# Kernel tuning notes

Measured on AMD Instinct MI355X. Metric: run time of the kernel, lower is better.

The kernel has to match this reference:

```python
import jax, jax.numpy as jnp
import numpy as np
import math


def _fft_size(n: int) -> int:
    return max(2 * 2 ** int(math.ceil(math.log2(n))), 16)


def setup_inputs() -> dict:
    key = jax.random.key(0)
    k1, k2 = jax.random.split(key)
    b, n, d = 4, 8192, 512
    x = jax.random.normal(k1, (b, n, d), dtype=jnp.float32)
    t = jax.random.normal(k2, (n, d), dtype=jnp.float32)
    return {"x": x, "t": t}


def reference(x, t):
    # x: (b, n, d); t: (n, d) Toeplitz coefficients t0..t_{n-1} per channel.
    # o[b, i, d] = gelu( sum_{j<=i} t[i-j, d] * x[b, j, d] )
    # computed via zero-padded real FFT of size >= 2n (causal linear conv).
    b, n, d = x.shape
    N = _fft_size(n)  # 2 * next_pow2(n)
    t_f = jnp.fft.rfft(t, n=N, axis=0)          # (N//2+1, d) complex
    x_f = jnp.fft.rfft(x, n=N, axis=1)          # (b, N//2+1, d) complex
    y = jnp.fft.irfft(x_f * t_f[None], n=N, axis=1)[:, :n, :]  # (b, n, d)
    return jax.nn.gelu(y)
```

## Files before the change

### kernel.cpp

```cpp
#include <hip/hip_runtime.h>
#include <hip/hip_bf16.h>

typedef short short8 __attribute__((ext_vector_type(8)));
typedef float f32x4  __attribute__((ext_vector_type(4)));

#define N_SEQ 8192
#define D_CH  512

constexpr int XSLOTS  = 1280;
constexpr int XLDS_B  = XSLOTS * 8;
constexpr int TSTRIDE = 272;
constexpr int TLDS_B  = 8 * TSTRIDE;
constexpr int ALL_LDS = XLDS_B + TLDS_B;

__device__ __forceinline__ unsigned short f32_to_bf16_bits(float f) {
    union { float f; unsigned int u; } v; v.f = f;
    unsigned int u = v.u;
    unsigned int r = u + 0x7FFFu + ((u >> 16) & 1u);
    return (unsigned short)(r >> 16);
}

__device__ __forceinline__ float gelu_f(float v) {
  float w = v * (2.3022031f + 0.10294296f * v * v);
  float e = __builtin_amdgcn_exp2f(w);
  float r = __builtin_amdgcn_rcpf(e + 1.0f);
  return v - v * r;
}

__global__ __launch_bounds__(256) void transpose_cast_kernel(
    const float* __restrict__ x, const float* __restrict__ t,
    unsigned short* __restrict__ xT, unsigned short* __restrict__ tT) {
  __shared__ float tile[64][65];
  int blk = blockIdx.x;
  int bat = blk >> 10;
  int rem = blk & 1023;
  int i0 = (rem >> 3) << 6;
  int d0 = (rem & 7) << 6;
  const float* src; unsigned short* dst;
  if (bat < 4) { src = x + (size_t)bat * N_SEQ * D_CH; dst = xT + (size_t)bat * D_CH * N_SEQ; }
  else         { src = t;                              dst = tT; }
  int tx = threadIdx.x & 63, ty = threadIdx.x >> 6;
  #pragma unroll
  for (int r = ty; r < 64; r += 4)
    tile[r][tx] = src[(size_t)(i0 + r) * D_CH + (d0 + tx)];
  __syncthreads();
  #pragma unroll
  for (int r = ty; r < 64; r += 4)
    dst[(size_t)(d0 + r) * N_SEQ + (i0 + tx)] = f32_to_bf16_bits(tile[tx][r]);
}

__global__ __launch_bounds__(256) void transpose_out_kernel(
    const float* __restrict__ src, float* __restrict__ dst) {
  __shared__ float tile[64][65];
  int blk = blockIdx.x;
  int b   = blk >> 10;
  int rem = blk & 1023;
  int d0 = (rem & 7) << 6;
  int i0 = (rem >> 3) << 6;
  int tx = threadIdx.x & 63, ty = threadIdx.x >> 6;
  #pragma unroll
  for (int r = ty; r < 64; r += 4)
    tile[r][tx] = src[((size_t)(d0 + r) * 4 + b) * N_SEQ + i0 + tx];
  __syncthreads();
  #pragma unroll
  for (int r = ty; r < 64; r += 4)
    dst[((size_t)b * N_SEQ + i0 + r) * D_CH + d0 + tx] = tile[tx][r];
}

template<int DMAJOR>
__global__ __launch_bounds__(64, 3) void tno_conv_kernel(
    const unsigned short* __restrict__ xT, const unsigned short* __restrict__ tT,
    float* __restrict__ outp) {
  __shared__ __align__(16) char lds[ALL_LDS];
  const int lane = threadIdx.x & 63;
  const int blk  = blockIdx.x;
  const int d    = blk & 511;
  const int strip = 7 - (blk >> 9);
  const int base  = strip << 10;
  const int l_hi  = base + 960;

  const int m      = lane & 15;
  const int kb     = (lane >> 4) << 3;
  const int bcol   = m & 3;
  const int sl     = m >> 2;
  const int rA     = m & 7;
  const int aConst = kb - (m & 8);
  char* ldsX = lds;
  char* ldsT = lds + XLDS_B;
  const char* tb = ldsT + rA * TSTRIDE;
  const int stJ  = lane & 31;
  const int stR0 = (lane >> 5) << 2;
  const unsigned short* tTd = tT + ((size_t)d << 13);
  const int uLin = (lane & 3) | ((lane >> 4) << 2);
  const int sb   = (lane >> 2) & 3;
  const unsigned short* xlaneB = xT + (((size_t)sb * D_CH + d) << 13) + (uLin << 1);

  typedef __attribute__((address_space(3))) unsigned int lds_u32;
  typedef const __attribute__((address_space(1))) unsigned int glb_u32;

  f32x4 acc[4][4];
  #pragma unroll
  for (int g = 0; g < 4; ++g)
    #pragma unroll
    for (int k = 0; k < 4; ++k)
      acc[g][k] = (f32x4){0.f, 0.f, 0.f, 0.f};

  unsigned short tp0 = tTd[l_hi + 32 + stJ];
  unsigned short tp1 = tTd[l_hi + stJ];
  unsigned short tp2 = tTd[l_hi - 32 + stJ];
  asm volatile("" ::: "memory");

  {
    f32x4 z = (f32x4){0.f, 0.f, 0.f, 0.f};
    #pragma unroll
    for (int j = 0; j < 7; ++j)
      *(f32x4*)(ldsX + 2560 + (j << 10) + (lane << 4)) = z;
    *(unsigned long long*)(ldsX + 9728 + (lane << 3)) = 0ull;
    #pragma unroll
    for (int j = 0; j < 8; ++j)
      __builtin_amdgcn_global_load_lds((glb_u32*)(const void*)(xlaneB + (j << 5)),
                                       (lds_u32*)(void*)(ldsX + (j << 8)), 4, 0, 0);
  }
  asm volatile("" ::: "memory");

  #pragma unroll
  for (int c = 0; c < 4; ++c) {
    int r = stR0 + c;
    char* cw = ldsT + r * TSTRIDE;
    *(unsigned short*)(cw + (((r - (l_hi + 32 + stJ)) & 127) << 1)) = tp0;
    *(unsigned short*)(cw + (((r - (l_hi      + stJ)) & 127) << 1)) = tp1;
    *(unsigned short*)(cw + (((r - (l_hi - 32 + stJ)) & 127) << 1)) = tp2;
  }

  unsigned short tv[8];
  #pragma unroll
  for (int u = 0; u < 8; ++u)
    tv[u] = tTd[l_hi - 32 * u - 63 + stJ];

  asm volatile("s_waitcnt vmcnt(0)" ::: "memory");

  int aC = ((aConst - l_hi) & 127) << 1;
  short8 af2 = *(const short8*)(tb + ((aC - 64) & 255));
  short8 af3 = *(const short8*)(tb + ((aC - 96) & 255));
  int xo[4];
  #pragma unroll
  for (int g = 0; g < 4; ++g) {
    int row = (base - l_hi) + (g << 8) + (sl << 6) + kb;
    int slot = row + ((row < 0) ? XSLOTS : 0);
    xo[g] = (slot << 3) + (bcol << 4);
  }
  int twb[4];
  #pragma unroll
  for (int c = 0; c < 4; ++c)
    twb[c] = (((stR0 + c) - (l_hi - 63 + stJ)) & 127) << 1;
  int tgi = l_hi - 319 + stJ;
  const unsigned short* xsp = xlaneB + 256;
  int wb = 256 << 3;

#define CONV_ITER(GMIN, U)                                                       \
  {                                                                              \
    asm volatile("s_waitcnt vmcnt(14)" ::: "memory");                            \
    short8 af0 = *(const short8*)(tb + aC);                                      \
    short8 af1 = *(const short8*)(tb + ((aC - 32) & 255));                       \
    __builtin_amdgcn_global_load_lds((glb_u32*)(const void*)xsp,                 \
        (lds_u32*)(void*)(ldsX + wb), 4, 0, 0);                                  \
    __builtin_amdgcn_s_setprio(1);                                               \
    _Pragma("unroll")                                                            \
    for (int g = 0; g < 4; ++g) {                                                \
      if (g >= (GMIN)) {                                                         \
        short8 bf = *(const short8*)(ldsX + xo[g]);                              \
        acc[g][0] = __builtin_amdgcn_mfma_f32_16x16x32_bf16(af0, bf, acc[g][0], 0, 0, 0); \
        acc[g][1] = __builtin_amdgcn_mfma_f32_16x16x32_bf16(af1, bf, acc[g][1], 0, 0, 0); \
        acc[g][2] = __builtin_amdgcn_mfma_f32_16x16x32_bf16(af2, bf, acc[g][2], 0, 0, 0); \
        acc[g][3] = __builtin_amdgcn_mfma_f32_16x16x32_bf16(af3, bf, acc[g][3], 0, 0, 0); \
      }                                                                          \
      xo[g] += 256; if (xo[g] >= XLDS_B) xo[g] -= XLDS_B;                        \
    }                                                                            \
    __builtin_amdgcn_s_setprio(0);                                               \
    { unsigned short tvs = tv[U];                                                \
      _Pragma("unroll")                                                          \
      for (int c = 0; c < 4; ++c) {                                              \
        *(unsigned short*)(ldsT + (stR0 + c) * TSTRIDE + twb[c]) = tvs;          \
        twb[c] = (twb[c] + 64) & 255;                                            \
      }                                                                          \
    }                                                                            \
    { int ti = (tgi < 0) ? 0 : tgi;                                              \
      unsigned short v = tTd[ti];               \
      tv[U] = (tgi < 0) ? (unsigned short)0 : v;                                 \
      tgi -= 32; }                                                               \
    af2 = af0; af3 = af1;                                                        \
    aC = (aC + 64) & 255;                                                        \
    xsp += 32;                                                                   \
    wb += 256; if (wb >= XLDS_B) wb -= XLDS_B;                                   \
  }

#define PH8(GMIN)                                                                \
    { _Pragma("unroll")                                                          \
      for (int u = 0; u < 8; ++u) CONV_ITER(GMIN, u) }

  PH8(3)
  PH8(2)
  PH8(1)
  const int n0 = (strip << 2) + 1;
  #pragma unroll 1
  for (int c8 = 0; c8 < n0; ++c8)
    PH8(0)
#undef PH8
#undef CONV_ITER

  asm volatile("s_waitcnt vmcnt(0)" ::: "memory");

  if (DMAJOR) {
    float* op = outp + ((((size_t)d << 2) + bcol) << 13) + base + (sl << 6) + ((lane >> 4) << 2);
    #pragma unroll
    for (int g = 0; g < 4; ++g)
      #pragma unroll
      for (int k = 0; k < 4; ++k)
        #pragma unroll
        for (int r = 0; r < 4; ++r)
          op[(g << 8) + (k << 4) + r] = gelu_f(acc[g][k][r]);
  } else {
    #pragma unroll
    for (int g = 0; g < 4; ++g)
      #pragma unroll
      for (int k = 0; k < 4; ++k)
        #pragma unroll
        for (int r = 0; r < 4; ++r) {
          int i = base + (((g << 2) + sl) << 6) + (k << 4) + ((lane >> 4) << 2) + r;
          outp[(((size_t)bcol << 13) + (size_t)i) * D_CH + d] = gelu_f(acc[g][k][r]);
        }
  }
}

extern "C" void kernel_launch(void* const* d_in, const int* in_sizes, int n_in,
                              void* d_out, int out_size, void* d_ws, size_t ws_size,
                              hipStream_t stream) {
  const float* x = (const float*)d_in[0];
  const float* t = (const float*)d_in[1];
  float* out = (float*)d_out;

  const size_t xT_elems = (size_t)4 * D_CH * N_SEQ;
  const size_t tT_elems = (size_t)D_CH * N_SEQ;
  unsigned short* xT = (unsigned short*)d_ws;
  unsigned short* tT = xT + xT_elems;
  float* ows = (float*)(tT + tT_elems);
  const size_t need = xT_elems * 2 + tT_elems * 2 + (size_t)4 * N_SEQ * D_CH * 4;
  const bool dmaj = (ws_size >= need);

  hipLaunchKernelGGL(transpose_cast_kernel, dim3(5 * 1024), dim3(256), 0, stream,
                     x, t, xT, tT);
  if (dmaj) {
    hipLaunchKernelGGL((tno_conv_kernel<1>), dim3(4096), dim3(64), 0, stream,
                       xT, tT, ows);
    hipLaunchKernelGGL(transpose_out_kernel, dim3(4096), dim3(256), 0, stream,
                       ows, out);
  } else {
    hipLaunchKernelGGL((tno_conv_kernel<0>), dim3(4096), dim3(64), 0, stream,
                       xT, tT, out);
  }
}
```

Before: 165.9 us.

## Widen Toeplitz A-fragment reuse to 8 k-blocks and store intermediate in bf16

The conv kernel now keeps eight shifted Toeplitz fragments (af0..af7) per x fragment instead of four, and uses 2 row groups of 8 accumulator tiles instead of 4x4. Each B fragment loaded from LDS therefore feeds more MFMAs. The T LDS ring is doubled, the X ring gets an XOR swizzle to spread bank conflicts, and the load addressing is adjusted to match. The d-major intermediate is written as bf16 instead of fp32 to halve its memory traffic, at the cost of extra output rounding error and more live registers, which could hurt occupancy.

Measured after the change: 183.0 us. 10.3% more time.

```diff
diff --git a/kernel.cpp b/kernel.cpp
--- a/kernel.cpp
+++ b/kernel.cpp
@@ -3,13 +3,14 @@
 
 typedef short short8 __attribute__((ext_vector_type(8)));
 typedef float f32x4  __attribute__((ext_vector_type(4)));
+typedef unsigned short us4 __attribute__((ext_vector_type(4)));
 
 #define N_SEQ 8192
 #define D_CH  512
 
 constexpr int XSLOTS  = 1280;
 constexpr int XLDS_B  = XSLOTS * 8;
-constexpr int TSTRIDE = 272;
+constexpr int TSTRIDE = 544;
 constexpr int TLDS_B  = 8 * TSTRIDE;
 constexpr int ALL_LDS = XLDS_B + TLDS_B;
 
@@ -19,7 +20,9 @@
     unsigned int r = u + 0x7FFFu + ((u >> 16) & 1u);
     return (unsigned short)(r >> 16);
 }
-
+__device__ __forceinline__ float bf16_to_f32(unsigned short u) {
+  union { unsigned int u; float f; } v; v.u = ((unsigned int)u) << 16; return v.f;
+}
 __device__ __forceinline__ float gelu_f(float v) {
   float w = v * (2.3022031f + 0.10294296f * v * v);
   float e = __builtin_amdgcn_exp2f(w);
@@ -50,7 +53,7 @@
 }
 
 __global__ __launch_bounds__(256) void transpose_out_kernel(
-    const float* __restrict__ src, float* __restrict__ dst) {
+    const unsigned short* __restrict__ src, float* __restrict__ dst) {
   __shared__ float tile[64][65];
   int blk = blockIdx.x;
   int b   = blk >> 10;
@@ -60,7 +63,7 @@
   int tx = threadIdx.x & 63, ty = threadIdx.x >> 6;
   #pragma unroll
   for (int r = ty; r < 64; r += 4)
-    tile[r][tx] = src[((size_t)(d0 + r) * 4 + b) * N_SEQ + i0 + tx];
+    tile[r][tx] = bf16_to_f32(src[((size_t)(d0 + r) * 4 + b) * N_SEQ + i0 + tx]);
   __syncthreads();
   #pragma unroll
   for (int r = ty; r < 64; r += 4)
@@ -70,14 +73,14 @@
 template<int DMAJOR>
 __global__ __launch_bounds__(64, 3) void tno_conv_kernel(
     const unsigned short* __restrict__ xT, const unsigned short* __restrict__ tT,
-    float* __restrict__ outp) {
+    unsigned short* __restrict__ owsp, float* __restrict__ outp) {
   __shared__ __align__(16) char lds[ALL_LDS];
   const int lane = threadIdx.x & 63;
   const int blk  = blockIdx.x;
   const int d    = blk & 511;
   const int strip = 7 - (blk >> 9);
   const int base  = strip << 10;
-  const int l_hi  = base + 960;
+  const int l_hi  = base + 896;
 
   const int m      = lane & 15;
   const int kb     = (lane >> 4) << 3;
@@ -91,35 +94,38 @@
   const int stJ  = lane & 31;
   const int stR0 = (lane >> 5) << 2;
   const unsigned short* tTd = tT + ((size_t)d << 13);
+  const int sb   = (lane >> 2) & 3;
   const int uLin = (lane & 3) | ((lane >> 4) << 2);
-  const int sb   = (lane >> 2) & 3;
   const unsigned short* xlaneB = xT + (((size_t)sb * D_CH + d) << 13) + (uLin << 1);
+  const int rowAdj = ((lane >> 4) & 1) ? -8 : 8;
+  const int batAdj = (sb & 2) ? -8388608 : 8388608;
 
   typedef __attribute__((address_space(3))) unsigned int lds_u32;
   typedef const __attribute__((address_space(1))) unsigned int glb_u32;
 
-  f32x4 acc[4][4];
-  #pragma unroll
-  for (int g = 0; g < 4; ++g)
-    #pragma unroll
-    for (int k = 0; k < 4; ++k)
+  f32x4 acc[2][8];
+  #pragma unroll
+  for (int g = 0; g < 2; ++g)
+    #pragma unroll
+    for (int k = 0; k < 8; ++k)
       acc[g][k] = (f32x4){0.f, 0.f, 0.f, 0.f};
 
-  unsigned short tp0 = tTd[l_hi + 32 + stJ];
-  unsigned short tp1 = tTd[l_hi + stJ];
-  unsigned short tp2 = tTd[l_hi - 32 + stJ];
+  unsigned short tp[5];
+  #pragma unroll
+  for (int q = 0; q < 5; ++q)
+    tp[q] = tTd[l_hi + 96 - (q << 5) + stJ];
   asm volatile("" ::: "memory");
 
   {
     f32x4 z = (f32x4){0.f, 0.f, 0.f, 0.f};
     #pragma unroll
-    for (int j = 0; j < 7; ++j)
-      *(f32x4*)(ldsX + 2560 + (j << 10) + (lane << 4)) = z;
-    *(unsigned long long*)(ldsX + 9728 + (lane << 3)) = 0ull;
+    for (int j = 0; j < 3; ++j)
+      *(f32x4*)(ldsX + 7168 + (j << 10) + (lane << 4)) = z;
     #pragma unroll
     for (int j = 0; j < 8; ++j)
-      __builtin_amdgcn_global_load_lds((glb_u32*)(const void*)(xlaneB + (j << 5)),
-                                       (lds_u32*)(void*)(ldsX + (j << 8)), 4, 0, 0);
+      __builtin_amdgcn_global_load_lds(
+          (glb_u32*)(const void*)(xlaneB + (j << 5) + ((j & 4) ? rowAdj : 0)),
+          (lds_u32*)(void*)(ldsX + (j << 8)), 4, 0, 0);
   }
   asm volatile("" ::: "memory");
 
@@ -127,52 +133,66 @@
   for (int c = 0; c < 4; ++c) {
     int r = stR0 + c;
     char* cw = ldsT + r * TSTRIDE;
-    *(unsigned short*)(cw + (((r - (l_hi + 32 + stJ)) & 127) << 1)) = tp0;
-    *(unsigned short*)(cw + (((r - (l_hi      + stJ)) & 127) << 1)) = tp1;
-    *(unsigned short*)(cw + (((r - (l_hi - 32 + stJ)) & 127) << 1)) = tp2;
+    #pragma unroll
+    for (int q = 0; q < 5; ++q) {
+      int idx = l_hi + 96 - (q << 5) + stJ;
+      *(unsigned short*)(cw + (((r - idx) & 255) << 1)) = tp[q];
+    }
   }
 
   unsigned short tv[8];
   #pragma unroll
   for (int u = 0; u < 8; ++u)
-    tv[u] = tTd[l_hi - 32 * u - 63 + stJ];
+    tv[u] = tTd[l_hi - 63 - (u << 5) + stJ];
 
   asm volatile("s_waitcnt vmcnt(0)" ::: "memory");
 
-  int aC = ((aConst - l_hi) & 127) << 1;
-  short8 af2 = *(const short8*)(tb + ((aC - 64) & 255));
-  short8 af3 = *(const short8*)(tb + ((aC - 96) & 255));
-  int xo[4];
-  #pragma unroll
-  for (int g = 0; g < 4; ++g) {
-    int row = (base - l_hi) + (g << 8) + (sl << 6) + kb;
-    int slot = row + ((row < 0) ? XSLOTS : 0);
-    xo[g] = (slot << 3) + (bcol << 4);
+  int aC = ((aConst - l_hi) & 255) << 1;
+  short8 af0, af1;
+  short8 af2 = *(const short8*)(tb + ((aC - 64)  & 511));
+  short8 af3 = *(const short8*)(tb + ((aC - 96)  & 511));
+  short8 af4 = *(const short8*)(tb + ((aC - 128) & 511));
+  short8 af5 = *(const short8*)(tb + ((aC - 160) & 511));
+  short8 af6 = *(const short8*)(tb + ((aC - 192) & 511));
+  short8 af7 = *(const short8*)(tb + ((aC - 224) & 511));
+  int xo[2];
+  #pragma unroll
+  for (int g = 0; g < 2; ++g) {
+    int row = (base - l_hi) + (g << 9) + (sl << 7) + kb;
+    if (row < 0) row += XSLOTS;
+    xo[g] = (row << 3) + (bcol << 4);
   }
   int twb[4];
   #pragma unroll
   for (int c = 0; c < 4; ++c)
-    twb[c] = (((stR0 + c) - (l_hi - 63 + stJ)) & 127) << 1;
+    twb[c] = (((stR0 + c) - (l_hi - 63 + stJ)) & 255) << 1;
   int tgi = l_hi - 319 + stJ;
   const unsigned short* xsp = xlaneB + 256;
-  int wb = 256 << 3;
+  int wb = 2048;
 
 #define CONV_ITER(GMIN, U)                                                       \
   {                                                                              \
     asm volatile("s_waitcnt vmcnt(14)" ::: "memory");                            \
-    short8 af0 = *(const short8*)(tb + aC);                                      \
-    short8 af1 = *(const short8*)(tb + ((aC - 32) & 255));                       \
-    __builtin_amdgcn_global_load_lds((glb_u32*)(const void*)xsp,                 \
-        (lds_u32*)(void*)(ldsX + wb), 4, 0, 0);                                  \
+    af0 = *(const short8*)(tb + aC);                                             \
+    af1 = *(const short8*)(tb + ((aC - 32) & 511));                              \
+    { const unsigned short* xs = xsp + ((wb & 1024) ? rowAdj : 0)                \
+                                     + ((wb & 2048) ? batAdj : 0);               \
+      __builtin_amdgcn_global_load_lds((glb_u32*)(const void*)xs,                \
+          (lds_u32*)(void*)(ldsX + wb), 4, 0, 0); }                              \
     __builtin_amdgcn_s_setprio(1);                                               \
     _Pragma("unroll")                                                            \
-    for (int g = 0; g < 4; ++g) {                                                \
+    for (int g = 0; g < 2; ++g) {                                                \
       if (g >= (GMIN)) {                                                         \
-        short8 bf = *(const short8*)(ldsX + xo[g]);                              \
+        int xsw = xo[g] ^ ((xo[g] & 1024) >> 4) ^ ((xo[g] & 2048) >> 6);         \
+        short8 bf = *(const short8*)(ldsX + xsw);                                \
         acc[g][0] = __builtin_amdgcn_mfma_f32_16x16x32_bf16(af0, bf, acc[g][0], 0, 0, 0); \
         acc[g][1] = __builtin_amdgcn_mfma_f32_16x16x32_bf16(af1, bf, acc[g][1], 0, 0, 0); \
         acc[g][2] = __builtin_amdgcn_mfma_f32_16x16x32_bf16(af2, bf, acc[g][2], 0, 0, 0); \
         acc[g][3] = __builtin_amdgcn_mfma_f32_16x16x32_bf16(af3, bf, acc[g][3], 0, 0, 0); \
+        acc[g][4] = __builtin_amdgcn_mfma_f32_16x16x32_bf16(af4, bf, acc[g][4], 0, 0, 0); \
+        acc[g][5] = __builtin_amdgcn_mfma_f32_16x16x32_bf16(af5, bf, acc[g][5], 0, 0, 0); \
+        acc[g][6] = __builtin_amdgcn_mfma_f32_16x16x32_bf16(af6, bf, acc[g][6], 0, 0, 0); \
+        acc[g][7] = __builtin_amdgcn_mfma_f32_16x16x32_bf16(af7, bf, acc[g][7], 0, 0, 0); \
       }                                                                          \
       xo[g] += 256; if (xo[g] >= XLDS_B) xo[g] -= XLDS_B;                        \
     }                                                                            \
@@ -181,15 +201,15 @@
       _Pragma("unroll")                                                          \
       for (int c = 0; c < 4; ++c) {                                              \
         *(unsigned short*)(ldsT + (stR0 + c) * TSTRIDE + twb[c]) = tvs;          \
-        twb[c] = (twb[c] + 64) & 255;                                            \
+        twb[c] = (twb[c] + 64) & 511;                                            \
       }                                                                          \
     }                                                                            \
     { int ti = (tgi < 0) ? 0 : tgi;                                              \
       unsigned short v = tTd[ti];               \
       tv[U] = (tgi < 0) ? (unsigned short)0 : v;                                 \
       tgi -= 32; }                                                               \
-    af2 = af0; af3 = af1;                                                        \
-    aC = (aC + 64) & 255;                                                        \
+    af7 = af5; af6 = af4; af5 = af3; af4 = af2; af3 = af1; af2 = af0;            \
+    aC = (aC + 64) & 511;                                                        \
     xsp += 32;                                                                   \
     wb += 256; if (wb >= XLDS_B) wb -= XLDS_B;                                   \
   }
@@ -198,10 +218,9 @@
     { _Pragma("unroll")                                                          \
       for (int u = 0; u < 8; ++u) CONV_ITER(GMIN, u) }
 
-  PH8(3)
-  PH8(2)
   PH8(1)
-  const int n0 = (strip << 2) + 1;
+  PH8(1)
+  const int n0 = (strip << 2) + 2;
   #pragma unroll 1
   for (int c8 = 0; c8 < n0; ++c8)
     PH8(0)
@@ -211,22 +230,26 @@
   asm volatile("s_waitcnt vmcnt(0)" ::: "memory");
 
   if (DMAJOR) {
-    float* op = outp + ((((size_t)d << 2) + bcol) << 13) + base + (sl << 6) + ((lane >> 4) << 2);
-    #pragma unroll
-    for (int g = 0; g < 4; ++g)
+    unsigned short* op = owsp + ((((size_t)d << 2) + bcol) << 13) + base
+                       + (sl << 7) + ((lane >> 4) << 2);
+    #pragma unroll
+    for (int g = 0; g < 2; ++g)
       #pragma unroll
-      for (int k = 0; k < 4; ++k)
+      for (int k = 0; k < 8; ++k) {
+        us4 w;
         #pragma unroll
         for (int r = 0; r < 4; ++r)
-          op[(g << 8) + (k << 4) + r] = gelu_f(acc[g][k][r]);
+          w[r] = f32_to_bf16_bits(gelu_f(acc[g][k][r]));
+        *(us4*)(op + (g << 9) + (k << 4)) = w;
+      }
   } else {
     #pragma unroll
-    for (int g = 0; g < 4; ++g)
+    for (int g = 0; g < 2; ++g)
       #pragma unroll
-      for (int k = 0; k < 4; ++k)
+      for (int k = 0; k < 8; ++k)
         #pragma unroll
         for (int r = 0; r < 4; ++r) {
-          int i = base + (((g << 2) + sl) << 6) + (k << 4) + ((lane >> 4) << 2) + r;
+          int i = base + (g << 9) + (sl << 7) + (k << 4) + ((lane >> 4) << 2) + r;
           outp[(((size_t)bcol << 13) + (size_t)i) * D_CH + d] = gelu_f(acc[g][k][r]);
         }
   }
@@ -241,21 +264,21 @@
 
   const size_t xT_elems = (size_t)4 * D_CH * N_SEQ;
   const size_t tT_elems = (size_t)D_CH * N_SEQ;
-  unsigned short* xT = (unsigned short*)d_ws;
-  unsigned short* tT = xT + xT_elems;
-  float* ows = (float*)(tT + tT_elems);
-  const size_t need = xT_elems * 2 + tT_elems * 2 + (size_t)4 * N_SEQ * D_CH * 4;
+  unsigned short* xT  = (unsigned short*)d_ws;
+  unsigned short* tT  = xT + xT_elems;
+  unsigned short* ows = tT + tT_elems;
+  const size_t need = (xT_elems + tT_elems + xT_elems) * 2;
   const bool dmaj = (ws_size >= need);
 
   hipLaunchKernelGGL(transpose_cast_kernel, dim3(5 * 1024), dim3(256), 0, stream,
                      x, t, xT, tT);
   if (dmaj) {
     hipLaunchKernelGGL((tno_conv_kernel<1>), dim3(4096), dim3(64), 0, stream,
-                       xT, tT, ows);
+                       xT, tT, ows, out);
     hipLaunchKernelGGL(transpose_out_kernel, dim3(4096), dim3(256), 0, stream,
                        ows, out);
   } else {
     hipLaunchKernelGGL((tno_conv_kernel<0>), dim3(4096), dim3(64), 0, stream,
-                       xT, tT, out);
-  }
-}
+                       xT, tT, ows, out);
+  }
+}
```

## Deepen x prefetch ring and store intermediate conv output as bf16

Applied to the files above, without the earlier changes.

Enlarges the LDS ring buffer for x from 1280 to 1536 slots, and raises the in-flight global-to-LDS loads and t prefetch registers from 8 to 16 iterations, loosening the vmcnt wait, so memory latency is hidden further ahead. The main loop is restructured into alternating 8-iteration halves to index the larger tv register array. The d-major intermediate buffer becomes bf16 instead of fp32, halving the bytes written by the conv kernel and read by the output transpose. This adds LDS and register pressure, which may lower occupancy, and rounds post-GELU outputs to bf16, reducing accuracy.

Result: slower. 170.5 us (+2.8%).

```diff
diff --git a/kernel.cpp b/kernel.cpp
--- a/kernel.cpp
+++ b/kernel.cpp
@@ -3,11 +3,12 @@
 
 typedef short short8 __attribute__((ext_vector_type(8)));
 typedef float f32x4  __attribute__((ext_vector_type(4)));
+typedef unsigned short us4 __attribute__((ext_vector_type(4)));
 
 #define N_SEQ 8192
 #define D_CH  512
 
-constexpr int XSLOTS  = 1280;
+constexpr int XSLOTS  = 1536;
 constexpr int XLDS_B  = XSLOTS * 8;
 constexpr int TSTRIDE = 272;
 constexpr int TLDS_B  = 8 * TSTRIDE;
@@ -19,7 +20,9 @@
     unsigned int r = u + 0x7FFFu + ((u >> 16) & 1u);
     return (unsigned short)(r >> 16);
 }
-
+__device__ __forceinline__ float bf16_to_f32(unsigned short u) {
+  union { unsigned int u; float f; } v; v.u = ((unsigned int)u) << 16; return v.f;
+}
 __device__ __forceinline__ float gelu_f(float v) {
   float w = v * (2.3022031f + 0.10294296f * v * v);
   float e = __builtin_amdgcn_exp2f(w);
@@ -50,7 +53,7 @@
 }
 
 __global__ __launch_bounds__(256) void transpose_out_kernel(
-    const float* __restrict__ src, float* __restrict__ dst) {
+    const unsigned short* __restrict__ src, float* __restrict__ dst) {
   __shared__ float tile[64][65];
   int blk = blockIdx.x;
   int b   = blk >> 10;
@@ -60,7 +63,7 @@
   int tx = threadIdx.x & 63, ty = threadIdx.x >> 6;
   #pragma unroll
   for (int r = ty; r < 64; r += 4)
-    tile[r][tx] = src[((size_t)(d0 + r) * 4 + b) * N_SEQ + i0 + tx];
+    tile[r][tx] = bf16_to_f32(src[((size_t)(d0 + r) * 4 + b) * N_SEQ + i0 + tx]);
   __syncthreads();
   #pragma unroll
   for (int r = ty; r < 64; r += 4)
@@ -70,7 +73,7 @@
 template<int DMAJOR>
 __global__ __launch_bounds__(64, 3) void tno_conv_kernel(
     const unsigned short* __restrict__ xT, const unsigned short* __restrict__ tT,
-    float* __restrict__ outp) {
+    unsigned short* __restrict__ owsp, float* __restrict__ outp) {
   __shared__ __align__(16) char lds[ALL_LDS];
   const int lane = threadIdx.x & 63;
   const int blk  = blockIdx.x;
@@ -114,10 +117,10 @@
     f32x4 z = (f32x4){0.f, 0.f, 0.f, 0.f};
     #pragma unroll
     for (int j = 0; j < 7; ++j)
-      *(f32x4*)(ldsX + 2560 + (j << 10) + (lane << 4)) = z;
-    *(unsigned long long*)(ldsX + 9728 + (lane << 3)) = 0ull;
-    #pragma unroll
-    for (int j = 0; j < 8; ++j)
+      *(f32x4*)(ldsX + 4608 + (j << 10) + (lane << 4)) = z;
+    *(unsigned long long*)(ldsX + 11776 + (lane << 3)) = 0ull;
+    #pragma unroll
+    for (int j = 0; j < 16; ++j)
       __builtin_amdgcn_global_load_lds((glb_u32*)(const void*)(xlaneB + (j << 5)),
                                        (lds_u32*)(void*)(ldsX + (j << 8)), 4, 0, 0);
   }
@@ -132,34 +135,35 @@
     *(unsigned short*)(cw + (((r - (l_hi - 32 + stJ)) & 127) << 1)) = tp2;
   }
 
-  unsigned short tv[8];
-  #pragma unroll
-  for (int u = 0; u < 8; ++u)
-    tv[u] = tTd[l_hi - 32 * u - 63 + stJ];
-
-  asm volatile("s_waitcnt vmcnt(0)" ::: "memory");
+  unsigned short tv[16];
+  #pragma unroll
+  for (int u = 0; u < 16; ++u)
+    tv[u] = tTd[l_hi - 63 - (u << 5) + stJ];
 
   int aC = ((aConst - l_hi) & 127) << 1;
-  short8 af2 = *(const short8*)(tb + ((aC - 64) & 255));
-  short8 af3 = *(const short8*)(tb + ((aC - 96) & 255));
+  short8 af2, af3;
+  {
+    af2 = *(const short8*)(tb + ((aC - 64) & 255));
+    af3 = *(const short8*)(tb + ((aC - 96) & 255));
+  }
   int xo[4];
   #pragma unroll
   for (int g = 0; g < 4; ++g) {
     int row = (base - l_hi) + (g << 8) + (sl << 6) + kb;
-    int slot = row + ((row < 0) ? XSLOTS : 0);
-    xo[g] = (slot << 3) + (bcol << 4);
+    if (row < 0) row += XSLOTS;
+    xo[g] = (row << 3) + (bcol << 4);
   }
   int twb[4];
   #pragma unroll
   for (int c = 0; c < 4; ++c)
     twb[c] = (((stR0 + c) - (l_hi - 63 + stJ)) & 127) << 1;
-  int tgi = l_hi - 319 + stJ;
-  const unsigned short* xsp = xlaneB + 256;
-  int wb = 256 << 3;
+  int tgi = l_hi - 575 + stJ;
+  const unsigned short* xsp = xlaneB + 512;
+  int wb = 4096;
 
 #define CONV_ITER(GMIN, U)                                                       \
   {                                                                              \
-    asm volatile("s_waitcnt vmcnt(14)" ::: "memory");                            \
+    asm volatile("s_waitcnt vmcnt(30)" ::: "memory");                            \
     short8 af0 = *(const short8*)(tb + aC);                                      \
     short8 af1 = *(const short8*)(tb + ((aC - 32) & 255));                       \
     __builtin_amdgcn_global_load_lds((glb_u32*)(const void*)xsp,                 \
@@ -194,31 +198,37 @@
     wb += 256; if (wb >= XLDS_B) wb -= XLDS_B;                                   \
   }
 
-#define PH8(GMIN)                                                                \
+#define PH8(GMIN, UB)                                                            \
     { _Pragma("unroll")                                                          \
-      for (int u = 0; u < 8; ++u) CONV_ITER(GMIN, u) }
-
-  PH8(3)
-  PH8(2)
-  PH8(1)
-  const int n0 = (strip << 2) + 1;
+      for (int u = 0; u < 8; ++u) CONV_ITER(GMIN, (UB) + u) }
+
+  PH8(3, 0)
+  PH8(2, 8)
+  PH8(1, 0)
   #pragma unroll 1
-  for (int c8 = 0; c8 < n0; ++c8)
-    PH8(0)
+  for (int i2 = 0; i2 < (strip << 1); ++i2) {
+    PH8(0, 8)
+    PH8(0, 0)
+  }
+  PH8(0, 8)
 #undef PH8
 #undef CONV_ITER
 
   asm volatile("s_waitcnt vmcnt(0)" ::: "memory");
 
   if (DMAJOR) {
-    float* op = outp + ((((size_t)d << 2) + bcol) << 13) + base + (sl << 6) + ((lane >> 4) << 2);
+    unsigned short* op = owsp + ((((size_t)d << 2) + bcol) << 13) + base
+                       + (sl << 6) + ((lane >> 4) << 2);
     #pragma unroll
     for (int g = 0; g < 4; ++g)
       #pragma unroll
-      for (int k = 0; k < 4; ++k)
+      for (int k = 0; k < 4; ++k) {
+        us4 w;
         #pragma unroll
         for (int r = 0; r < 4; ++r)
-          op[(g << 8) + (k << 4) + r] = gelu_f(acc[g][k][r]);
+          w[r] = f32_to_bf16_bits(gelu_f(acc[g][k][r]));
+        *(us4*)(op + (g << 8) + (k << 4)) = w;
+      }
   } else {
     #pragma unroll
     for (int g = 0; g < 4; ++g)
@@ -241,21 +251,21 @@
 
   const size_t xT_elems = (size_t)4 * D_CH * N_SEQ;
   const size_t tT_elems = (size_t)D_CH * N_SEQ;
-  unsigned short* xT = (unsigned short*)d_ws;
-  unsigned short* tT = xT + xT_elems;
-  float* ows = (float*)(tT + tT_elems);
-  const size_t need = xT_elems * 2 + tT_elems * 2 + (size_t)4 * N_SEQ * D_CH * 4;
+  unsigned short* xT  = (unsigned short*)d_ws;
+  unsigned short* tT  = xT + xT_elems;
+  unsigned short* ows = tT + tT_elems;
+  const size_t need = (xT_elems + tT_elems + xT_elems) * 2;
   const bool dmaj = (ws_size >= need);
 
   hipLaunchKernelGGL(transpose_cast_kernel, dim3(5 * 1024), dim3(256), 0, stream,
                      x, t, xT, tT);
   if (dmaj) {
     hipLaunchKernelGGL((tno_conv_kernel<1>), dim3(4096), dim3(64), 0, stream,
-                       xT, tT, ows);
+                       xT, tT, ows, out);
     hipLaunchKernelGGL(transpose_out_kernel, dim3(4096), dim3(256), 0, stream,
                        ows, out);
   } else {
     hipLaunchKernelGGL((tno_conv_kernel<0>), dim3(4096), dim3(64), 0, stream,
-                       xT, tT, out);
-  }
-}
+                       xT, tT, ows, out);
+  }
+}
```
